# Kernel optimization log

Hardware: AMD Instinct MI355X
Metric: run time of the kernel (lower is better)

The kernel has to match this reference:

```python
import jax, jax.numpy as jnp
import numpy as np

B, T, I, H, O = 256, 256, 16, 256, 11
HYP_HID = 512
BLD = 8
N1 = H * I + H * H + 2 * H        # RNN cell params (W_ih, W_hh, b_ih, b_hh)
N2 = O * H + O                    # readout params (W_out, b_out)


def setup_inputs() -> dict:
    key = jax.random.key(0)
    k = jax.random.split(key, 4)
    bld = jax.random.normal(k[0], (B, BLD), dtype=jnp.float32)
    stimulus = jax.random.normal(k[1], (B, T, I), dtype=jnp.float32)
    # hypnet MLP: bld -> relu -> flat per-sample params; small init to keep tanh unsaturated
    W1 = jax.random.normal(k[2], (BLD, HYP_HID), dtype=jnp.float32) * 0.05
    b1 = jnp.zeros((HYP_HID,), dtype=jnp.float32)
    W2 = jax.random.normal(k[3], (HYP_HID, N1 + N2), dtype=jnp.float32) * 0.02
    b2 = jnp.zeros((N1 + N2,), dtype=jnp.float32)
    return {"bld": bld, "stimulus": stimulus, "W1": W1, "b1": b1, "W2": W2, "b2": b2}


def reference(bld, stimulus, W1, b1, W2, b2):
    # hypernetwork: per-sample flat params [B, N1+N2]
    flat = jax.nn.relu(bld @ W1 + b1) @ W2 + b2
    params1, params2 = flat[:, :N1], flat[:, N1:]

    # unpack per-sample RNN cell params
    o = 0
    W_ih = params1[:, o:o + H * I].reshape(B, H, I); o += H * I
    W_hh = params1[:, o:o + H * H].reshape(B, H, H); o += H * H
    b_ih = params1[:, o:o + H]; o += H
    b_hh = params1[:, o:o + H]
    W_out = params2[:, :O * H].reshape(B, O, H)
    b_out = params2[:, O * H:].reshape(B, O)

    # shift stimulus right by one step with a zero frame (teacher forcing input)
    rnn_input = jnp.concatenate(
        [jnp.zeros((B, 1, I), dtype=stimulus.dtype), stimulus[:, :-1]], axis=1)

    # precompute input projection for all steps: [B, T, H]
    x_proj = jnp.einsum('bti,bhi->bth', rnn_input, W_ih) + b_ih[:, None, :]

    def step(h, xp_t):  # h: [B, H], xp_t: [B, H]
        h_next = jnp.tanh(xp_t + jnp.einsum('bh,bgh->bg', h, W_hh) + b_hh)
        return h_next, h_next

    h0 = jnp.zeros((B, H), dtype=stimulus.dtype)
    h_last, out_tm = jax.lax.scan(step, h0, jnp.swapaxes(x_proj, 0, 1))
    output1 = jnp.swapaxes(out_tm, 0, 1)  # [B, T, H]

    # per-sample linear readout [B, T, O]
    output2 = jnp.einsum('bth,boh->bto', output1, W_out) + b_out[:, None, :]
    output2 = jnp.nan_to_num(output2, nan=0.0)

    output_act = jax.nn.sigmoid(output2[:, :, :3])
    output_bldi = output2[:, :, 3:]
    h = h_last[None]  # [1, B, H]
    return (output_act, output_bldi, h, params1, params2)
```

## Files before the change

### kernel.cpp

```cpp
#include <hip/hip_runtime.h>

typedef unsigned short u16;
typedef unsigned int u32;
using short8   = __attribute__((ext_vector_type(8))) short;
using floatx4  = __attribute__((ext_vector_type(4))) float;
using half_t   = _Float16;
using half2_t  = __attribute__((ext_vector_type(2))) _Float16;
using halfx8   = __attribute__((ext_vector_type(8))) _Float16;

constexpr int B_ = 256, T_ = 256, I_ = 16, H_ = 256, O_ = 11;
constexpr int HYP = 512;
constexpr int N1_ = H_ * I_ + H_ * H_ + 2 * H_;
constexpr int N2_ = O_ * H_ + O_;
constexpr int GN  = N1_ + N2_;

constexpr size_t OUT_ACT  = 0;
constexpr size_t OUT_BLDI = (size_t)B_ * T_ * 3;
constexpr size_t OUT_H    = OUT_BLDI + (size_t)B_ * T_ * 8;
constexpr size_t OUT_P1   = OUT_H + (size_t)B_ * H_;
constexpr size_t OUT_P2   = OUT_P1 + (size_t)B_ * N1_;

__device__ inline void bar_lds() {
    asm volatile("s_waitcnt lgkmcnt(0)\n\ts_barrier" ::: "memory");
}

__device__ inline float bf2f(u16 u) {
    union { u32 i; float f; } v; v.i = ((u32)u) << 16; return v.f;
}
__device__ inline u16 f2bf(float f) {
    u32 x = __float_as_uint(f);
    u32 r = (x + 0x7fffu + ((x >> 16) & 1u)) >> 16;
    return (u16)r;
}
__device__ inline float fdot2(half2_t a, half2_t b, float c) {
#if __has_builtin(__builtin_amdgcn_fdot2)
    return __builtin_amdgcn_fdot2(a, b, c, false);
#else
    return c + (float)a.x * (float)b.x + (float)a.y * (float)b.y;
#endif
}

union H8 { halfx8 v; half2_t h2[4]; };

__device__ inline bool sniff_f32(const void* p) {
    const u16* w = (const u16*)p;
    const int lane = threadIdx.x & 63;
    u16 u = w[lane * 2];
    unsigned e = (u >> 7) & 0xFF;
    bool inband = (u == 0) || (e >= 77 && e <= 140);
    return __popcll(__ballot(inband)) < 56;
}

__device__ inline float ldr(const void* p, size_t i, bool f32) {
    return f32 ? ((const float*)p)[i] : bf2f(((const u16*)p)[i]);
}

__global__ void h1_kernel(const void* __restrict__ bld, const void* __restrict__ W1,
                          const void* __restrict__ b1, u16* __restrict__ h1) {
    const bool bldf = sniff_f32(bld);
    const bool w1f  = sniff_f32(W1);
    const bool b1f  = sniff_f32(b1);
    const int b = blockIdx.x;
    const int j = threadIdx.x;
    float acc = ldr(b1, j, b1f);
#pragma unroll
    for (int k = 0; k < 8; k++)
        acc += ldr(bld, b * 8 + k, bldf) * ldr(W1, k * HYP + j, w1f);
    h1[b * HYP + j] = f2bf(fmaxf(acc, 0.f));
}

constexpr int KS_ = 32;
constexpr int NST = HYP / KS_;
constexpr int TKP = 40;

template<bool W2F32>
__device__ void gemm_body(const u16* __restrict__ A, const void* __restrict__ Bm,
                          const void* __restrict__ b2, bool b2f,
                          float* __restrict__ out) {
    __shared__ alignas(16) u16 tileT[64][TKP];

    const int nb   = blockIdx.x * 64;
    const int tid  = threadIdx.x;
    const int lane = tid & 63;
    const int wid  = tid >> 6;
    const int l15  = lane & 15;
    const int q    = lane >> 4;

    int  col[4]; bool cv[4];
#pragma unroll
    for (int j = 0; j < 4; j++) {
        int c = nb + j * 16 + l15;
        cv[j]  = (c < GN);
        col[j] = cv[j] ? c : (GN - 1);
    }

    const u16* ap[4];
#pragma unroll
    for (int i = 0; i < 4; i++)
        ap[i] = A + (wid * 64 + i * 16 + l15) * HYP + q * 8;

    const int scol_i = tid & 63;
    const int kq     = tid >> 6;
    int gc = nb + scol_i;
    if (gc >= GN) gc = GN - 1;
    const size_t colOff = (size_t)gc;

    float pf[8]; u16 pb[8];
    {
#pragma unroll
        for (int e = 0; e < 8; e++) {
            const size_t ro = (size_t)(kq * 8 + e) * (size_t)GN + colOff;
            if constexpr (W2F32) pf[e] = ((const float*)Bm)[ro];
            else                 pb[e] = ((const u16*)Bm)[ro];
        }
    }

    floatx4 acc[4][4] = {};

    for (int ks = 0; ks < NST; ks++) {
        short8 wv8;
#pragma unroll
        for (int e = 0; e < 8; e++) {
            if constexpr (W2F32) wv8[e] = (short)f2bf(pf[e]);
            else                 wv8[e] = (short)pb[e];
        }
        *(short8*)&tileT[scol_i][kq * 8] = wv8;

        if (ks + 1 < NST) {
#pragma unroll
            for (int e = 0; e < 8; e++) {
                const size_t ro = (size_t)((ks + 1) * KS_ + kq * 8 + e) * (size_t)GN + colOff;
                if constexpr (W2F32) pf[e] = ((const float*)Bm)[ro];
                else                 pb[e] = ((const u16*)Bm)[ro];
            }
        }
        bar_lds();

        short8 af[4];
#pragma unroll
        for (int i = 0; i < 4; i++)
            af[i] = *(const short8*)(ap[i] + ks * KS_);

        short8 bfr[4];
#pragma unroll
        for (int j = 0; j < 4; j++)
            bfr[j] = *(const short8*)&tileT[j * 16 + l15][q * 8];

#pragma unroll
        for (int i = 0; i < 4; i++)
#pragma unroll
            for (int j = 0; j < 4; j++)
                acc[i][j] = __builtin_amdgcn_mfma_f32_16x16x32_bf16(af[i], bfr[j], acc[i][j], 0, 0, 0);
        bar_lds();
    }

    const bool isP2 = (nb >= N1_);
#pragma unroll
    for (int j = 0; j < 4; j++) {
        const float bias = ldr(b2, col[j], b2f);
#pragma unroll
        for (int i = 0; i < 4; i++) {
            const int mbase = wid * 64 + i * 16 + q * 4;
#pragma unroll
            for (int r = 0; r < 4; r++) {
                if (cv[j]) {
                    const float v = acc[i][j][r] + bias;
                    const int m = mbase + r;
                    size_t dst;
                    if (isP2) dst = OUT_P2 + (size_t)m * N2_ + (size_t)(col[j] - N1_);
                    else      dst = OUT_P1 + (size_t)m * N1_ + (size_t)col[j];
                    out[dst] = v;
                }
            }
        }
    }
}
__global__ __launch_bounds__(256) void gemm_kernel(const u16* A, const void* Bm,
                                                   const void* b2, float* out) {
    const bool w2f = sniff_f32(Bm);
    const bool b2f = sniff_f32(b2);
    if (w2f) gemm_body<true>(A, Bm, b2, b2f, out);
    else     gemm_body<false>(A, Bm, b2, b2f, out);
}

constexpr int ROWH = 264;

__global__ __launch_bounds__(512) void rnn_kernel(const void* __restrict__ stim,
                                                  float* __restrict__ out) {
    const bool stf = sniff_f32(stim);
    const int b    = blockIdx.x;
    const int tid  = threadIdx.x;
    const int lane = tid & 63;
    const int wv   = tid >> 6;
    const int g    = wv * 32 + (lane >> 1);
    const int hf   = lane & 1;

    const float* p1 = out + OUT_P1 + (size_t)b * N1_;
    const float* p2 = out + OUT_P2 + (size_t)b * N2_;

    __shared__ alignas(16) half_t  hist[(T_ + 1) * ROWH];
    __shared__ alignas(16) half2_t stim_s[T_ * 8];
    __shared__ alignas(16) half_t  wo_s[O_ * ROWH];

    if (stf) {
        const float2* sp = (const float2*)stim + (size_t)b * T_ * 8;
        for (int idx = tid; idx < T_ * 8; idx += 512) {
            float2 v = sp[idx];
            half2_t h; h.x = (half_t)v.x; h.y = (half_t)v.y;
            stim_s[idx] = h;
        }
    } else {
        const u32* sp = (const u32*)((const u16*)stim + (size_t)b * T_ * I_);
        for (int idx = tid; idx < T_ * 8; idx += 512) {
            u32 u = sp[idx];
            union { u32 i; float f; } lo2, hi2;
            lo2.i = u << 16; hi2.i = u & 0xffff0000u;
            half2_t h; h.x = (half_t)lo2.f; h.y = (half_t)hi2.f;
            stim_s[idx] = h;
        }
    }

    half2_t Wr[64];
    {
        const float4* wp4 = (const float4*)(p1 + H_ * I_ + (size_t)g * H_ + hf * 128);
#pragma unroll
        for (int v = 0; v < 32; v++) {
            float4 r4 = wp4[v];
            half2_t h01, h23;
            h01.x = (half_t)r4.x; h01.y = (half_t)r4.y;
            h23.x = (half_t)r4.z; h23.y = (half_t)r4.w;
            Wr[v * 2 + 0] = h01;
            Wr[v * 2 + 1] = h23;
        }
    }

    half2_t Wih[8];
    float bc = 0.f;
    if (!hf) {
        const float4* ip = (const float4*)(p1 + (size_t)g * I_);
#pragma unroll
        for (int v = 0; v < 4; v++) {
            float4 r4 = ip[v];
            half2_t h01, h23;
            h01.x = (half_t)r4.x; h01.y = (half_t)r4.y;
            h23.x = (half_t)r4.z; h23.y = (half_t)r4.w;
            Wih[v * 2 + 0] = h01;
            Wih[v * 2 + 1] = h23;
        }
        bc = p1[H_ * I_ + H_ * H_ + g] + p1[H_ * I_ + H_ * H_ + H_ + g];
    }

    for (int idx = tid; idx < ROWH / 2; idx += 512)
        ((u32*)hist)[idx] = 0u;
    __syncthreads();

    const int goff = g + ((g >= 128) ? 8 : 0);

    for (int t = 0; t < T_; t++) {
        const half_t* hrow = hist + (size_t)t * ROWH;
        const halfx8* hv8  = (const halfx8*)(hrow + hf * 136);

        float a0 = 0.f, a1 = 0.f, a2 = 0.f, a3 = 0.f;
#pragma unroll
        for (int c = 0; c < 16; c++) {
            H8 u; u.v = hv8[c];
            a0 = fdot2(Wr[c * 4 + 0], u.h2[0], a0);
            a1 = fdot2(Wr[c * 4 + 1], u.h2[1], a1);
            a2 = fdot2(Wr[c * 4 + 2], u.h2[2], a2);
            a3 = fdot2(Wr[c * 4 + 3], u.h2[3], a3);
        }
        float part = (a0 + a1) + (a2 + a3);

        if (!hf) {
            float xa = bc;
            if (t > 0) {
                const halfx8* sp8 = (const halfx8*)(&stim_s[(t - 1) * 8]);
                H8 u0, u1; u0.v = sp8[0]; u1.v = sp8[1];
                xa = fdot2(Wih[0], u0.h2[0], xa);
                xa = fdot2(Wih[1], u0.h2[1], xa);
                xa = fdot2(Wih[2], u0.h2[2], xa);
                xa = fdot2(Wih[3], u0.h2[3], xa);
                xa = fdot2(Wih[4], u1.h2[0], xa);
                xa = fdot2(Wih[5], u1.h2[1], xa);
                xa = fdot2(Wih[6], u1.h2[2], xa);
                xa = fdot2(Wih[7], u1.h2[3], xa);
            }
            part += xa;
        }
        part += __shfl_xor(part, 1);

        if (!hf) {
            const float e  = __expf(2.f * part);
            const float hn = 1.f - 2.f / (e + 1.f);
            hist[(size_t)(t + 1) * ROWH + goff] = (half_t)hn;
            if (t == T_ - 1) out[OUT_H + (size_t)b * H_ + g] = hn;
        }
        bar_lds();
    }

    __syncthreads();
    for (int idx = tid; idx < O_ * H_; idx += 512) {
        const int o = idx >> 8, c = idx & 255;
        wo_s[o * ROWH + c + ((c >= 128) ? 8 : 0)] = (half_t)p2[idx];
    }
    __syncthreads();

    {
        const int t   = tid & 255;
        const int par = tid >> 8;
        const half_t* hr_ = hist + (size_t)(t + 1) * ROWH;

        halfx8 hv[32];
        {
            const halfx8* h8a = (const halfx8*)hr_;
            const halfx8* h8b = (const halfx8*)(hr_ + 136);
#pragma unroll
            for (int c = 0; c < 16; c++) hv[c] = h8a[c];
#pragma unroll
            for (int c = 0; c < 16; c++) hv[16 + c] = h8b[c];
        }

        const size_t act_base  = OUT_ACT  + (size_t)b * T_ * 3 + (size_t)t * 3;
        const size_t bldi_base = OUT_BLDI + (size_t)b * T_ * 8 + (size_t)t * 8;

        for (int o = par; o < O_; o += 2) {
            const halfx8* w8a = (const halfx8*)(wo_s + o * ROWH);
            const halfx8* w8b = (const halfx8*)(wo_s + o * ROWH + 136);
            float d0 = 0.f, d1 = 0.f, d2 = 0.f, d3 = 0.f;
#pragma unroll
            for (int c = 0; c < 16; c++) {
                H8 hu, wu; hu.v = hv[c]; wu.v = w8a[c];
                d0 = fdot2(wu.h2[0], hu.h2[0], d0);
                d1 = fdot2(wu.h2[1], hu.h2[1], d1);
                d2 = fdot2(wu.h2[2], hu.h2[2], d2);
                d3 = fdot2(wu.h2[3], hu.h2[3], d3);
            }
#pragma unroll
            for (int c = 0; c < 16; c++) {
                H8 hu, wu; hu.v = hv[16 + c]; wu.v = w8b[c];
                d0 = fdot2(wu.h2[0], hu.h2[0], d0);
                d1 = fdot2(wu.h2[1], hu.h2[1], d1);
                d2 = fdot2(wu.h2[2], hu.h2[2], d2);
                d3 = fdot2(wu.h2[3], hu.h2[3], d3);
            }
            float v2 = (d0 + d1) + (d2 + d3) + p2[O_ * H_ + o];
            if (o < 3) out[act_base + o] = 1.f / (1.f + __expf(-v2));
            else       out[bldi_base + (o - 3)] = v2;
        }
    }
}

extern "C" void kernel_launch(void* const* d_in, const int* in_sizes, int n_in,
                              void* d_out, int out_size, void* d_ws, size_t ws_size,
                              hipStream_t stream) {
    (void)in_sizes; (void)n_in; (void)out_size; (void)d_ws; (void)ws_size;
    const void* bld  = d_in[0];
    const void* stim = d_in[1];
    const void* W1   = d_in[2];
    const void* b1   = d_in[3];
    const void* W2   = d_in[4];
    const void* b2   = d_in[5];
    float* out = (float*)d_out;
    u16* h1 = (u16*)out;

    h1_kernel<<<B_, HYP, 0, stream>>>(bld, W1, b1, h1);
    gemm_kernel<<<(GN + 63) / 64, 256, 0, stream>>>(h1, W2, b2, out);
    rnn_kernel<<<B_, 512, 0, stream>>>(stim, out);
}
```

Baseline: 455.0 us.

## Use MFMA for RNN recurrence and readout with fused input projection

Rewrites the per-step recurrent matvec from fdot2 over 512 threads into 16x16x32 f16 MFMA over 256 threads, with W_hh held as MFMA B-fragments in registers. The input projection and bias are folded into a ninth K-tile by padding the shifted stimulus with a constant-one column. The readout also moves to MFMA over blocks of 16 timesteps. Only one of the 16 MFMA output columns is useful in the recurrence, so most tensor work is wasted, and the large register footprint forces one block per CU.

Result: no change. 452.8 us (-0.5%).

```diff
diff --git a/kernel.cpp b/kernel.cpp
--- a/kernel.cpp
+++ b/kernel.cpp
@@ -32,15 +32,6 @@
     u32 r = (x + 0x7fffu + ((x >> 16) & 1u)) >> 16;
     return (u16)r;
 }
-__device__ inline float fdot2(half2_t a, half2_t b, float c) {
-#if __has_builtin(__builtin_amdgcn_fdot2)
-    return __builtin_amdgcn_fdot2(a, b, c, false);
-#else
-    return c + (float)a.x * (float)b.x + (float)a.y * (float)b.y;
-#endif
-}
-
-union H8 { halfx8 v; half2_t h2[4]; };
 
 __device__ inline bool sniff_f32(const void* p) {
     const u16* w = (const u16*)p;
@@ -183,169 +174,152 @@
     else     gemm_body<false>(A, Bm, b2, b2f, out);
 }
 
-constexpr int ROWH = 264;
-
-__global__ __launch_bounds__(512) void rnn_kernel(const void* __restrict__ stim,
-                                                  float* __restrict__ out) {
+constexpr int HROW = 256;
+constexpr int XROW = 40;
+
+__global__ __launch_bounds__(256, 1) void rnn_kernel(const void* __restrict__ stim,
+                                                     float* __restrict__ out) {
     const bool stf = sniff_f32(stim);
     const int b    = blockIdx.x;
     const int tid  = threadIdx.x;
     const int lane = tid & 63;
     const int wv   = tid >> 6;
-    const int g    = wv * 32 + (lane >> 1);
-    const int hf   = lane & 1;
+    const int l15  = lane & 15;
+    const int q    = lane >> 4;
 
     const float* p1 = out + OUT_P1 + (size_t)b * N1_;
     const float* p2 = out + OUT_P2 + (size_t)b * N2_;
 
-    __shared__ alignas(16) half_t  hist[(T_ + 1) * ROWH];
-    __shared__ alignas(16) half2_t stim_s[T_ * 8];
-    __shared__ alignas(16) half_t  wo_s[O_ * ROWH];
+    __shared__ alignas(16) half_t hist[(T_ + 1) * HROW];
+    __shared__ alignas(16) half_t stim_s[T_ * XROW];
 
     if (stf) {
         const float2* sp = (const float2*)stim + (size_t)b * T_ * 8;
-        for (int idx = tid; idx < T_ * 8; idx += 512) {
+        for (int idx = tid; idx < (T_ - 1) * 8; idx += 256) {
+            const int tt = idx >> 3, pr = idx & 7;
             float2 v = sp[idx];
             half2_t h; h.x = (half_t)v.x; h.y = (half_t)v.y;
-            stim_s[idx] = h;
+            *(half2_t*)&stim_s[(tt + 1) * XROW + pr * 2] = h;
         }
     } else {
         const u32* sp = (const u32*)((const u16*)stim + (size_t)b * T_ * I_);
-        for (int idx = tid; idx < T_ * 8; idx += 512) {
+        for (int idx = tid; idx < (T_ - 1) * 8; idx += 256) {
+            const int tt = idx >> 3, pr = idx & 7;
             u32 u = sp[idx];
             union { u32 i; float f; } lo2, hi2;
             lo2.i = u << 16; hi2.i = u & 0xffff0000u;
             half2_t h; h.x = (half_t)lo2.f; h.y = (half_t)hi2.f;
-            stim_s[idx] = h;
-        }
-    }
-
-    half2_t Wr[64];
+            *(half2_t*)&stim_s[(tt + 1) * XROW + pr * 2] = h;
+        }
+    }
     {
-        const float4* wp4 = (const float4*)(p1 + H_ * I_ + (size_t)g * H_ + hf * 128);
-#pragma unroll
-        for (int v = 0; v < 32; v++) {
-            float4 r4 = wp4[v];
-            half2_t h01, h23;
-            h01.x = (half_t)r4.x; h01.y = (half_t)r4.y;
-            h23.x = (half_t)r4.z; h23.y = (half_t)r4.w;
-            Wr[v * 2 + 0] = h01;
-            Wr[v * 2 + 1] = h23;
-        }
-    }
-
-    half2_t Wih[8];
-    float bc = 0.f;
-    if (!hf) {
-        const float4* ip = (const float4*)(p1 + (size_t)g * I_);
-#pragma unroll
-        for (int v = 0; v < 4; v++) {
-            float4 r4 = ip[v];
-            half2_t h01, h23;
-            h01.x = (half_t)r4.x; h01.y = (half_t)r4.y;
-            h23.x = (half_t)r4.z; h23.y = (half_t)r4.w;
-            Wih[v * 2 + 0] = h01;
-            Wih[v * 2 + 1] = h23;
-        }
-        bc = p1[H_ * I_ + H_ * H_ + g] + p1[H_ * I_ + H_ * H_ + H_ + g];
-    }
-
-    for (int idx = tid; idx < ROWH / 2; idx += 512)
-        ((u32*)hist)[idx] = 0u;
+        u32* ss = (u32*)stim_s;
+        const int base = tid * (XROW / 2);
+        ss[base + 8] = 0x00003C00u;
+#pragma unroll
+        for (int z = 9; z < XROW / 2; z++) ss[base + z] = 0u;
+        if (tid < 8)   ss[tid] = 0u;
+        if (tid < 128) ((u32*)hist)[tid] = 0u;
+    }
+
+    halfx8 Wf[4][9];
+    {
+        const float* WH  = p1 + H_ * I_;
+        const float* BIH = p1 + H_ * I_ + H_ * H_;
+#pragma unroll
+        for (int i = 0; i < 4; i++) {
+            const int rr = 64 * wv + i * 16 + l15;
+#pragma unroll
+            for (int kt = 0; kt < 8; kt++) {
+                const float4* wp = (const float4*)(WH + (size_t)rr * H_ + kt * 32 + q * 8);
+                float4 r0 = wp[0], r1 = wp[1];
+                halfx8 f;
+                f[0] = (half_t)r0.x; f[1] = (half_t)r0.y; f[2] = (half_t)r0.z; f[3] = (half_t)r0.w;
+                f[4] = (half_t)r1.x; f[5] = (half_t)r1.y; f[6] = (half_t)r1.z; f[7] = (half_t)r1.w;
+                Wf[i][kt] = f;
+            }
+            halfx8 fx;
+#pragma unroll
+            for (int j = 0; j < 8; j++) fx[j] = (half_t)0.f;
+            if (q < 2) {
+                const float4* ip = (const float4*)(p1 + (size_t)rr * I_ + q * 8);
+                float4 r0 = ip[0], r1 = ip[1];
+                fx[0] = (half_t)r0.x; fx[1] = (half_t)r0.y; fx[2] = (half_t)r0.z; fx[3] = (half_t)r0.w;
+                fx[4] = (half_t)r1.x; fx[5] = (half_t)r1.y; fx[6] = (half_t)r1.z; fx[7] = (half_t)r1.w;
+            } else if (q == 2) {
+                fx[0] = (half_t)(BIH[rr] + BIH[H_ + rr]);
+            }
+            Wf[i][8] = fx;
+        }
+    }
     __syncthreads();
 
-    const int goff = g + ((g >= 128) ? 8 : 0);
-
     for (int t = 0; t < T_; t++) {
-        const half_t* hrow = hist + (size_t)t * ROWH;
-        const halfx8* hv8  = (const halfx8*)(hrow + hf * 136);
-
-        float a0 = 0.f, a1 = 0.f, a2 = 0.f, a3 = 0.f;
-#pragma unroll
-        for (int c = 0; c < 16; c++) {
-            H8 u; u.v = hv8[c];
-            a0 = fdot2(Wr[c * 4 + 0], u.h2[0], a0);
-            a1 = fdot2(Wr[c * 4 + 1], u.h2[1], a1);
-            a2 = fdot2(Wr[c * 4 + 2], u.h2[2], a2);
-            a3 = fdot2(Wr[c * 4 + 3], u.h2[3], a3);
-        }
-        float part = (a0 + a1) + (a2 + a3);
-
-        if (!hf) {
-            float xa = bc;
-            if (t > 0) {
-                const halfx8* sp8 = (const halfx8*)(&stim_s[(t - 1) * 8]);
-                H8 u0, u1; u0.v = sp8[0]; u1.v = sp8[1];
-                xa = fdot2(Wih[0], u0.h2[0], xa);
-                xa = fdot2(Wih[1], u0.h2[1], xa);
-                xa = fdot2(Wih[2], u0.h2[2], xa);
-                xa = fdot2(Wih[3], u0.h2[3], xa);
-                xa = fdot2(Wih[4], u1.h2[0], xa);
-                xa = fdot2(Wih[5], u1.h2[1], xa);
-                xa = fdot2(Wih[6], u1.h2[2], xa);
-                xa = fdot2(Wih[7], u1.h2[3], xa);
-            }
-            part += xa;
-        }
-        part += __shfl_xor(part, 1);
-
-        if (!hf) {
-            const float e  = __expf(2.f * part);
+        halfx8 af[9];
+        const half_t* hr = hist + (size_t)t * HROW + q * 8;
+#pragma unroll
+        for (int kt = 0; kt < 8; kt++)
+            af[kt] = *(const halfx8*)(hr + kt * 32);
+        af[8] = *(const halfx8*)(stim_s + (size_t)t * XROW + q * 8);
+
+        floatx4 acc[4] = {};
+#pragma unroll
+        for (int kt = 0; kt < 9; kt++)
+#pragma unroll
+            for (int i = 0; i < 4; i++)
+                acc[i] = __builtin_amdgcn_mfma_f32_16x16x32_f16(af[kt], Wf[i][kt], acc[i], 0, 0, 0);
+
+        half_t* hw = hist + (size_t)(t + 1) * HROW;
+#pragma unroll
+        for (int i = 0; i < 4; i++) {
+            const float s  = acc[i][0];
+            const float e  = __expf(2.f * s);
             const float hn = 1.f - 2.f / (e + 1.f);
-            hist[(size_t)(t + 1) * ROWH + goff] = (half_t)hn;
-            if (t == T_ - 1) out[OUT_H + (size_t)b * H_ + g] = hn;
+            if (lane < 16) {
+                hw[64 * wv + i * 16 + l15] = (half_t)hn;
+                if (t == T_ - 1) out[OUT_H + (size_t)b * H_ + 64 * wv + i * 16 + l15] = hn;
+            }
         }
         bar_lds();
     }
 
-    __syncthreads();
-    for (int idx = tid; idx < O_ * H_; idx += 512) {
-        const int o = idx >> 8, c = idx & 255;
-        wo_s[o * ROWH + c + ((c >= 128) ? 8 : 0)] = (half_t)p2[idx];
-    }
-    __syncthreads();
-
+    halfx8 Wo[8];
+    float bo = 0.f;
     {
-        const int t   = tid & 255;
-        const int par = tid >> 8;
-        const half_t* hr_ = hist + (size_t)(t + 1) * ROWH;
-
-        halfx8 hv[32];
-        {
-            const halfx8* h8a = (const halfx8*)hr_;
-            const halfx8* h8b = (const halfx8*)(hr_ + 136);
-#pragma unroll
-            for (int c = 0; c < 16; c++) hv[c] = h8a[c];
-#pragma unroll
-            for (int c = 0; c < 16; c++) hv[16 + c] = h8b[c];
-        }
-
-        const size_t act_base  = OUT_ACT  + (size_t)b * T_ * 3 + (size_t)t * 3;
-        const size_t bldi_base = OUT_BLDI + (size_t)b * T_ * 8 + (size_t)t * 8;
-
-        for (int o = par; o < O_; o += 2) {
-            const halfx8* w8a = (const halfx8*)(wo_s + o * ROWH);
-            const halfx8* w8b = (const halfx8*)(wo_s + o * ROWH + 136);
-            float d0 = 0.f, d1 = 0.f, d2 = 0.f, d3 = 0.f;
-#pragma unroll
-            for (int c = 0; c < 16; c++) {
-                H8 hu, wu; hu.v = hv[c]; wu.v = w8a[c];
-                d0 = fdot2(wu.h2[0], hu.h2[0], d0);
-                d1 = fdot2(wu.h2[1], hu.h2[1], d1);
-                d2 = fdot2(wu.h2[2], hu.h2[2], d2);
-                d3 = fdot2(wu.h2[3], hu.h2[3], d3);
-            }
-#pragma unroll
-            for (int c = 0; c < 16; c++) {
-                H8 hu, wu; hu.v = hv[16 + c]; wu.v = w8b[c];
-                d0 = fdot2(wu.h2[0], hu.h2[0], d0);
-                d1 = fdot2(wu.h2[1], hu.h2[1], d1);
-                d2 = fdot2(wu.h2[2], hu.h2[2], d2);
-                d3 = fdot2(wu.h2[3], hu.h2[3], d3);
-            }
-            float v2 = (d0 + d1) + (d2 + d3) + p2[O_ * H_ + o];
-            if (o < 3) out[act_base + o] = 1.f / (1.f + __expf(-v2));
-            else       out[bldi_base + (o - 3)] = v2;
+#pragma unroll
+        for (int kt = 0; kt < 8; kt++) {
+            halfx8 f;
+#pragma unroll
+            for (int j = 0; j < 8; j++) f[j] = (half_t)0.f;
+            if (l15 < O_) {
+                const float* wp = p2 + (size_t)l15 * H_ + kt * 32 + q * 8;
+#pragma unroll
+                for (int j = 0; j < 8; j++) f[j] = (half_t)wp[j];
+            }
+            Wo[kt] = f;
+        }
+        if (l15 < O_) bo = p2[O_ * H_ + l15];
+    }
+
+#pragma unroll
+    for (int m = 0; m < 4; m++) {
+        const int tb = (4 * wv + m) * 16;
+        const half_t* hr = hist + (size_t)(tb + l15 + 1) * HROW + q * 8;
+        floatx4 acc = {};
+#pragma unroll
+        for (int kt = 0; kt < 8; kt++) {
+            halfx8 a = *(const halfx8*)(hr + kt * 32);
+            acc = __builtin_amdgcn_mfma_f32_16x16x32_f16(a, Wo[kt], acc, 0, 0, 0);
+        }
+        if (l15 < O_) {
+            const int o = l15;
+#pragma unroll
+            for (int r = 0; r < 4; r++) {
+                const int tt = tb + q * 4 + r;
+                float v2 = acc[r] + bo;
+                if (o < 3) out[OUT_ACT + (size_t)b * T_ * 3 + (size_t)tt * 3 + o] = 1.f / (1.f + __expf(-v2));
+                else       out[OUT_BLDI + (size_t)b * T_ * 8 + (size_t)tt * 8 + (o - 3)] = v2;
+            }
         }
     }
 }
@@ -365,5 +339,5 @@
 
     h1_kernel<<<B_, HYP, 0, stream>>>(bld, W1, b1, h1);
     gemm_kernel<<<(GN + 63) / 64, 256, 0, stream>>>(h1, W2, b2, out);
-    rnn_kernel<<<B_, 512, 0, stream>>>(stim, out);
-}
+    rnn_kernel<<<B_, 256, 0, stream>>>(stim, out);
+}
```
